# Performance work log

Measured on AMD Instinct MI355X. Metric: run time of the kernel, lower is better.

Reference implementation:

```python
import jax, jax.numpy as jnp
import numpy as np

HIDDEN = 1024
RANK = 4
INPUT = 16
ALPHA = 0.1
BASE_SCALE = 500.0
B = 32
T = 1024


def setup_inputs() -> dict:
    key = jax.random.key(0)
    k1, k2, k3, k4 = jax.random.split(key, 4)
    std = HIDDEN ** -0.25  # matches cov ~ I/sqrt(hidden) in original init
    x = jax.random.normal(k1, (B, T, INPUT), dtype=jnp.float32)
    m = jax.random.normal(k2, (HIDDEN, RANK), dtype=jnp.float32) * std
    n = jax.random.normal(k3, (HIDDEN, RANK), dtype=jnp.float32) * std
    I_mat = jax.random.normal(k4, (HIDDEN, INPUT), dtype=jnp.float32) * std
    return {"x": x, "m": m, "n": n, "I_mat": I_mat}


def reference(x, m, n, I_mat):
    # J = (m @ n.T) * base_scale / hidden ; recurrent term (J @ tanh(h).T).T
    # == tanh(h) @ J.T == ((tanh(h) @ n) @ m.T) * scale  (low-rank form, same math)
    scale = BASE_SCALE / HIDDEN

    def step(h, x_t):
        rec = (jnp.tanh(h) @ n) @ m.T * scale          # [B, H]
        dh = -h + rec + x_t @ I_mat.T                  # [B, H]
        h = h + ALPHA * dh
        return h, h

    h0 = jnp.zeros((x.shape[0], HIDDEN), dtype=x.dtype)
    _, hiddens = jax.lax.scan(step, h0, jnp.swapaxes(x, 0, 1))  # [T, B, H]
    hiddens = jnp.swapaxes(hiddens, 0, 1)                       # [B, T, H]

    span = jnp.concatenate([m, I_mat], axis=1)   # [H, RANK+INPUT]
    proj = jnp.linalg.pinv(span)                 # [RANK+INPUT, H]
    # (pinv(span) @ hiddens.permute(0,2,1)).permute(0,2,1)
    return jnp.einsum('ph,bth->btp', proj, hiddens)  # [B, T, RANK+INPUT]
```

## Files before the change

### kernel.cpp

```cpp
#include <hip/hip_runtime.h>
#include <math.h>

#define HIDDEN_ 1024
#define RANK_ 4
#define INPUT_ 16
#define T_ 1024
#define BATCH_ 32

#define NTHREADS_ 256
#define NWAVES_ (NTHREADS_ / 64)
#define EPT_ (HIDDEN_ / NTHREADS_)
#define CH_ 64
#define NCH_ (T_ / CH_)

typedef float f32x4 __attribute__((ext_vector_type(4)));

__device__ __forceinline__ float fast_exp2(float x) {
#if defined(__has_builtin)
#if __has_builtin(__builtin_amdgcn_exp2f)
    return __builtin_amdgcn_exp2f(x);
#else
    return exp2f(x);
#endif
#else
    return exp2f(x);
#endif
}

__device__ __forceinline__ float fast_rcp(float x) {
#if defined(__has_builtin)
#if __has_builtin(__builtin_amdgcn_rcpf)
    return __builtin_amdgcn_rcpf(x);
#else
    return 1.0f / x;
#endif
#else
    return 1.0f / x;
#endif
}

__device__ __forceinline__ float tanh_fast(float x) {
    float e = fast_exp2(x * 2.885390081777926815f);
    return fmaf(-2.0f, fast_rcp(e + 1.0f), 1.0f);
}

#define DPP_ADD(v, ctrl)                                                          \
    do {                                                                          \
        int _t = __builtin_amdgcn_update_dpp(0, __float_as_int(v), (ctrl), 0xf,   \
                                             0xf, true);                          \
        (v) += __int_as_float(_t);                                                \
    } while (0)

#define GLOAD16(dst, ptr)                                                         \
    asm volatile("global_load_dwordx4 %0, %1, off" : "=v"(dst) : "v"(ptr) : "memory")

__global__ __launch_bounds__(NTHREADS_)
__attribute__((amdgpu_waves_per_eu(1, 1)))
void rnn_scan_kernel(
    const float* __restrict__ x,
    const float* __restrict__ m,
    const float* __restrict__ n,
    const float* __restrict__ imat,
    float* __restrict__ out)
{
    const int b    = blockIdx.x;
    const int tid  = threadIdx.x;
    const int wave = tid >> 6;
    const int lane = tid & 63;

    const float kd   = 0.9f;
    const float krec = 0.1f * (500.0f / 1024.0f);
    const float kin  = 0.1f;

    f32x4 Iv[EPT_][4];
    f32x4 mv[EPT_];
    f32x4 nv[EPT_];
#pragma unroll
    for (int j = 0; j < EPT_; ++j) {
        const int hidx = tid * EPT_ + j;
        const float* ip = imat + hidx * INPUT_;
        GLOAD16(Iv[j][0], ip);
        GLOAD16(Iv[j][1], ip + 4);
        GLOAD16(Iv[j][2], ip + 8);
        GLOAD16(Iv[j][3], ip + 12);
        GLOAD16(mv[j], m + hidx * RANK_);
        GLOAD16(nv[j], n + hidx * RANK_);
    }
    asm volatile("s_waitcnt vmcnt(0)" ::: "memory");

    float h[EPT_];
    float mrs[EPT_][RANK_];
    float nr[EPT_][RANK_];
    float Irs[EPT_][INPUT_];
#pragma unroll
    for (int j = 0; j < EPT_; ++j) {
        h[j] = 0.0f;
#pragma unroll
        for (int r = 0; r < RANK_; ++r) {
            mrs[j][r] = krec * mv[j][r];
            nr[j][r]  = nv[j][r];
        }
#pragma unroll
        for (int q = 0; q < 4; ++q) {
#pragma unroll
            for (int e = 0; e < 4; ++e)
                Irs[j][q * 4 + e] = kin * Iv[j][q][e];
        }
    }

    __shared__ float4 part[2][NWAVES_];
    __shared__ float xs[2][CH_ * INPUT_];

    const float* xb = x + (size_t)b * T_ * INPUT_;
    float* ob = out + (size_t)b * T_ * (RANK_ + INPUT_);

    {
        float4 c0 = *(const float4*)(xb + tid * 4);
        *(float4*)&xs[0][tid * 4] = c0;
    }
    float4 xstage = *(const float4*)(xb + CH_ * INPUT_ + tid * 4);

    float y = 0.0f;
    const int yoff = (tid >= 4 && tid < 20) ? (tid - 4) : 0;

    for (int t = 0; t < T_; ++t) {
        float th[EPT_];
#pragma unroll
        for (int j = 0; j < EPT_; ++j) th[j] = tanh_fast(h[j]);

        float p0 = th[0] * nr[0][0], p1 = th[0] * nr[0][1];
        float p2 = th[0] * nr[0][2], p3 = th[0] * nr[0][3];
#pragma unroll
        for (int j = 1; j < EPT_; ++j) {
            p0 = fmaf(th[j], nr[j][0], p0);
            p1 = fmaf(th[j], nr[j][1], p1);
            p2 = fmaf(th[j], nr[j][2], p2);
            p3 = fmaf(th[j], nr[j][3], p3);
        }

        DPP_ADD(p0, 0x111); DPP_ADD(p1, 0x111); DPP_ADD(p2, 0x111); DPP_ADD(p3, 0x111);
        DPP_ADD(p0, 0x112); DPP_ADD(p1, 0x112); DPP_ADD(p2, 0x112); DPP_ADD(p3, 0x112);
        DPP_ADD(p0, 0x114); DPP_ADD(p1, 0x114); DPP_ADD(p2, 0x114); DPP_ADD(p3, 0x114);
        DPP_ADD(p0, 0x118); DPP_ADD(p1, 0x118); DPP_ADD(p2, 0x118); DPP_ADD(p3, 0x118);
        DPP_ADD(p0, 0x142); DPP_ADD(p1, 0x142); DPP_ADD(p2, 0x142); DPP_ADD(p3, 0x142);
        DPP_ADD(p0, 0x143); DPP_ADD(p1, 0x143); DPP_ADD(p2, 0x143); DPP_ADD(p3, 0x143);

        if (lane == 63) part[t & 1][wave] = make_float4(p0, p1, p2, p3);

        asm volatile("s_waitcnt lgkmcnt(0)\n\ts_barrier" ::: "memory");

        if ((t & (CH_ - 1)) == 0) {
            const int c = t >> 6;
            *(float4*)&xs[(c + 1) & 1][tid * 4] = xstage;
            const int cl = (c + 2 < NCH_) ? (c + 2) : (NCH_ - 1);
            xstage = *(const float4*)(xb + cl * CH_ * INPUT_ + tid * 4);
        }

        const float* xsp = &xs[(t >> 6) & 1][(t & 63) * INPUT_];
        const float4 xa = ((const float4*)xsp)[0];
        const float4 xbv = ((const float4*)xsp)[1];
        const float4 xc = ((const float4*)xsp)[2];
        const float4 xd = ((const float4*)xsp)[3];
        const float xyv = xsp[yoff];

        const float4 q0 = part[t & 1][0];
        const float4 q1 = part[t & 1][1];
        const float4 q2 = part[t & 1][2];
        const float4 q3 = part[t & 1][3];

        float ax[EPT_];
#pragma unroll
        for (int j = 0; j < EPT_; ++j) {
            float a = xa.x * Irs[j][0];
            float c = xa.y * Irs[j][1];
            a = fmaf(xa.z, Irs[j][2], a);   c = fmaf(xa.w, Irs[j][3], c);
            a = fmaf(xbv.x, Irs[j][4], a);  c = fmaf(xbv.y, Irs[j][5], c);
            a = fmaf(xbv.z, Irs[j][6], a);  c = fmaf(xbv.w, Irs[j][7], c);
            a = fmaf(xc.x, Irs[j][8], a);   c = fmaf(xc.y, Irs[j][9], c);
            a = fmaf(xc.z, Irs[j][10], a);  c = fmaf(xc.w, Irs[j][11], c);
            a = fmaf(xd.x, Irs[j][12], a);  c = fmaf(xd.y, Irs[j][13], c);
            a = fmaf(xd.z, Irs[j][14], a);  c = fmaf(xd.w, Irs[j][15], c);
            ax[j] = a + c;
        }

        const float s0 = (q0.x + q1.x) + (q2.x + q3.x);
        const float s1 = (q0.y + q1.y) + (q2.y + q3.y);
        const float s2 = (q0.z + q1.z) + (q2.z + q3.z);
        const float s3 = (q0.w + q1.w) + (q2.w + q3.w);

#pragma unroll
        for (int j = 0; j < EPT_; ++j) {
            float a01 = fmaf(s1, mrs[j][1], fmaf(s0, mrs[j][0], ax[j]));
            float a23 = fmaf(s3, mrs[j][3], s2 * mrs[j][2]);
            h[j] = fmaf(kd, h[j], a01 + a23);
        }

        if (tid < 20) {
            float drive;
            if (tid < 4) {
                float sv = (tid == 0) ? s0 : (tid == 1) ? s1 : (tid == 2) ? s2 : s3;
                drive = krec * sv;
            } else {
                drive = kin * xyv;
            }
            y = fmaf(kd, y, drive);
            ob[t * 20 + tid] = y;
        }
    }
}

extern "C" void kernel_launch(void* const* d_in, const int* in_sizes, int n_in,
                              void* d_out, int out_size, void* d_ws, size_t ws_size,
                              hipStream_t stream) {
    const float* x    = (const float*)d_in[0];
    const float* m    = (const float*)d_in[1];
    const float* n    = (const float*)d_in[2];
    const float* imat = (const float*)d_in[3];
    float* out = (float*)d_out;

    rnn_scan_kernel<<<dim3(BATCH_), dim3(NTHREADS_), 0, stream>>>(x, m, n, imat, out);
}
```

Measured before the change: 647.9 us.

## Precompute input projection in a parallel kernel and stream it into the scan

Adds a separate fully parallel kernel that computes the input drive x_t @ I^T for every batch row and timestep into a 128 MB workspace buffer. The sequential scan kernel then loads these values with a four-step register prefetch instead of doing 64 FMAs per thread per step. This moves work off the latency-bound serial path, at the cost of writing and re-reading a large intermediate through HBM. A fallback kernel keeps the old behaviour when the workspace is too small.

```diff
diff --git a/kernel.cpp b/kernel.cpp
--- a/kernel.cpp
+++ b/kernel.cpp
@@ -12,6 +12,10 @@
 #define EPT_ (HIDDEN_ / NTHREADS_)
 #define CH_ 64
 #define NCH_ (T_ / CH_)
+
+#define PRE_BLOCKS_ 2048
+#define ROWS_ (BATCH_ * T_)
+#define PASSES_ (ROWS_ / PRE_BLOCKS_)
 
 typedef float f32x4 __attribute__((ext_vector_type(4)));
 
@@ -51,8 +55,53 @@
         (v) += __int_as_float(_t);                                                \
     } while (0)
 
-#define GLOAD16(dst, ptr)                                                         \
-    asm volatile("global_load_dwordx4 %0, %1, off" : "=v"(dst) : "v"(ptr) : "memory")
+__global__ __launch_bounds__(NTHREADS_, 2) void precompute_u(
+    const float* __restrict__ x,
+    const float* __restrict__ imat,
+    float* __restrict__ u)
+{
+    const int tid = threadIdx.x;
+    const int bid = blockIdx.x;
+    const float kin = 0.1f;
+
+    float Ir[4][INPUT_];
+#pragma unroll
+    for (int r = 0; r < 4; ++r) {
+        const float* ip = imat + (4 * tid + r) * INPUT_;
+#pragma unroll
+        for (int q = 0; q < 4; ++q) {
+            const float4 v = *(const float4*)(ip + 4 * q);
+            Ir[r][q*4+0] = kin * v.x; Ir[r][q*4+1] = kin * v.y;
+            Ir[r][q*4+2] = kin * v.z; Ir[r][q*4+3] = kin * v.w;
+        }
+    }
+
+    for (int p = 0; p < PASSES_; ++p) {
+        const int row = p * PRE_BLOCKS_ + bid;
+        const float* xr = x + (size_t)row * INPUT_;
+        float xv[INPUT_];
+#pragma unroll
+        for (int q = 0; q < 4; ++q) {
+            const float4 v = ((const float4*)xr)[q];
+            xv[q*4+0] = v.x; xv[q*4+1] = v.y; xv[q*4+2] = v.z; xv[q*4+3] = v.w;
+        }
+        float4 acc;
+        float a[4];
+#pragma unroll
+        for (int r = 0; r < 4; ++r) {
+            float s0 = xv[0] * Ir[r][0];
+            float s1 = xv[1] * Ir[r][1];
+#pragma unroll
+            for (int i = 2; i < INPUT_; i += 2) {
+                s0 = fmaf(xv[i],     Ir[r][i],     s0);
+                s1 = fmaf(xv[i + 1], Ir[r][i + 1], s1);
+            }
+            a[r] = s0 + s1;
+        }
+        acc.x = a[0]; acc.y = a[1]; acc.z = a[2]; acc.w = a[3];
+        *(float4*)(u + (size_t)row * HIDDEN_ + 4 * tid) = acc;
+    }
+}
 
 __global__ __launch_bounds__(NTHREADS_)
 __attribute__((amdgpu_waves_per_eu(1, 1)))
@@ -60,7 +109,7 @@
     const float* __restrict__ x,
     const float* __restrict__ m,
     const float* __restrict__ n,
-    const float* __restrict__ imat,
+    const float* __restrict__ u,
     float* __restrict__ out)
 {
     const int b    = blockIdx.x;
@@ -70,48 +119,26 @@
 
     const float kd   = 0.9f;
     const float krec = 0.1f * (500.0f / 1024.0f);
-    const float kin  = 0.1f;
-
-    f32x4 Iv[EPT_][4];
-    f32x4 mv[EPT_];
-    f32x4 nv[EPT_];
-#pragma unroll
-    for (int j = 0; j < EPT_; ++j) {
-        const int hidx = tid * EPT_ + j;
-        const float* ip = imat + hidx * INPUT_;
-        GLOAD16(Iv[j][0], ip);
-        GLOAD16(Iv[j][1], ip + 4);
-        GLOAD16(Iv[j][2], ip + 8);
-        GLOAD16(Iv[j][3], ip + 12);
-        GLOAD16(mv[j], m + hidx * RANK_);
-        GLOAD16(nv[j], n + hidx * RANK_);
-    }
-    asm volatile("s_waitcnt vmcnt(0)" ::: "memory");
 
     float h[EPT_];
     float mrs[EPT_][RANK_];
     float nr[EPT_][RANK_];
-    float Irs[EPT_][INPUT_];
 #pragma unroll
     for (int j = 0; j < EPT_; ++j) {
+        const int hidx = tid * EPT_ + j;
         h[j] = 0.0f;
-#pragma unroll
-        for (int r = 0; r < RANK_; ++r) {
-            mrs[j][r] = krec * mv[j][r];
-            nr[j][r]  = nv[j][r];
-        }
-#pragma unroll
-        for (int q = 0; q < 4; ++q) {
-#pragma unroll
-            for (int e = 0; e < 4; ++e)
-                Irs[j][q * 4 + e] = kin * Iv[j][q][e];
-        }
+        const float4 mv = *(const float4*)(m + hidx * RANK_);
+        mrs[j][0] = krec * mv.x; mrs[j][1] = krec * mv.y;
+        mrs[j][2] = krec * mv.z; mrs[j][3] = krec * mv.w;
+        const float4 nv = *(const float4*)(n + hidx * RANK_);
+        nr[j][0] = nv.x; nr[j][1] = nv.y; nr[j][2] = nv.z; nr[j][3] = nv.w;
     }
 
     __shared__ float4 part[2][NWAVES_];
     __shared__ float xs[2][CH_ * INPUT_];
 
     const float* xb = x + (size_t)b * T_ * INPUT_;
+    const float* ub = u + (size_t)b * T_ * HIDDEN_ + tid * EPT_;
     float* ob = out + (size_t)b * T_ * (RANK_ + INPUT_);
 
     {
@@ -120,9 +147,15 @@
     }
     float4 xstage = *(const float4*)(xb + CH_ * INPUT_ + tid * 4);
 
+    float4 upf[4];
+#pragma unroll
+    for (int k = 0; k < 4; ++k)
+        upf[k] = *(const float4*)(ub + (size_t)k * HIDDEN_);
+
     float y = 0.0f;
     const int yoff = (tid >= 4 && tid < 20) ? (tid - 4) : 0;
 
+#pragma unroll 4
     for (int t = 0; t < T_; ++t) {
         float th[EPT_];
 #pragma unroll
@@ -156,18 +189,122 @@
             xstage = *(const float4*)(xb + cl * CH_ * INPUT_ + tid * 4);
         }
 
+        const float4 q0 = part[t & 1][0];
+        const float4 q1 = part[t & 1][1];
+        const float4 q2 = part[t & 1][2];
+        const float4 q3 = part[t & 1][3];
+        const float xyv = xs[(t >> 6) & 1][(t & 63) * INPUT_ + yoff];
+
+        const float4 uv = upf[t & 3];
+        {
+            const int tn = (t + 4 < T_) ? (t + 4) : t;
+            upf[t & 3] = *(const float4*)(ub + (size_t)tn * HIDDEN_);
+        }
+
+        const float s0 = (q0.x + q1.x) + (q2.x + q3.x);
+        const float s1 = (q0.y + q1.y) + (q2.y + q3.y);
+        const float s2 = (q0.z + q1.z) + (q2.z + q3.z);
+        const float s3 = (q0.w + q1.w) + (q2.w + q3.w);
+
+        const float uq[4] = {uv.x, uv.y, uv.z, uv.w};
+#pragma unroll
+        for (int j = 0; j < EPT_; ++j) {
+            float a01 = fmaf(s1, mrs[j][1], fmaf(s0, mrs[j][0], uq[j]));
+            float a23 = fmaf(s3, mrs[j][3], s2 * mrs[j][2]);
+            h[j] = fmaf(kd, h[j], a01 + a23);
+        }
+
+        if (tid < 20) {
+            float drive;
+            if (tid < 4) {
+                float sv = (tid == 0) ? s0 : (tid == 1) ? s1 : (tid == 2) ? s2 : s3;
+                drive = krec * sv;
+            } else {
+                drive = 0.1f * xyv;
+            }
+            y = fmaf(kd, y, drive);
+            ob[t * 20 + tid] = y;
+        }
+    }
+}
+
+__global__ __launch_bounds__(NTHREADS_)
+__attribute__((amdgpu_waves_per_eu(1, 1)))
+void rnn_scan_fallback(
+    const float* __restrict__ x, const float* __restrict__ m,
+    const float* __restrict__ n, const float* __restrict__ imat,
+    float* __restrict__ out)
+{
+    const int b    = blockIdx.x;
+    const int tid  = threadIdx.x;
+    const int wave = tid >> 6;
+    const int lane = tid & 63;
+    const float kd = 0.9f, krec = 0.1f * (500.0f / 1024.0f), kin = 0.1f;
+
+    float h[EPT_], mrs[EPT_][RANK_], nr[EPT_][RANK_], Irs[EPT_][INPUT_];
+#pragma unroll
+    for (int j = 0; j < EPT_; ++j) {
+        const int hidx = tid * EPT_ + j;
+        h[j] = 0.0f;
+        const float4 mv = *(const float4*)(m + hidx * RANK_);
+        mrs[j][0] = krec * mv.x; mrs[j][1] = krec * mv.y;
+        mrs[j][2] = krec * mv.z; mrs[j][3] = krec * mv.w;
+        const float4 nv = *(const float4*)(n + hidx * RANK_);
+        nr[j][0] = nv.x; nr[j][1] = nv.y; nr[j][2] = nv.z; nr[j][3] = nv.w;
+#pragma unroll
+        for (int q = 0; q < 4; ++q) {
+            const float4 iv = *(const float4*)(imat + hidx * INPUT_ + q * 4);
+            Irs[j][q*4+0] = kin * iv.x; Irs[j][q*4+1] = kin * iv.y;
+            Irs[j][q*4+2] = kin * iv.z; Irs[j][q*4+3] = kin * iv.w;
+        }
+    }
+    __shared__ float4 part[2][NWAVES_];
+    __shared__ float xs[2][CH_ * INPUT_];
+    const float* xb = x + (size_t)b * T_ * INPUT_;
+    float* ob = out + (size_t)b * T_ * (RANK_ + INPUT_);
+    {
+        float4 c0 = *(const float4*)(xb + tid * 4);
+        *(float4*)&xs[0][tid * 4] = c0;
+    }
+    float4 xstage = *(const float4*)(xb + CH_ * INPUT_ + tid * 4);
+    float y = 0.0f;
+    const int yoff = (tid >= 4 && tid < 20) ? (tid - 4) : 0;
+
+    for (int t = 0; t < T_; ++t) {
+        float th[EPT_];
+#pragma unroll
+        for (int j = 0; j < EPT_; ++j) th[j] = tanh_fast(h[j]);
+        float p0 = th[0] * nr[0][0], p1 = th[0] * nr[0][1];
+        float p2 = th[0] * nr[0][2], p3 = th[0] * nr[0][3];
+#pragma unroll
+        for (int j = 1; j < EPT_; ++j) {
+            p0 = fmaf(th[j], nr[j][0], p0); p1 = fmaf(th[j], nr[j][1], p1);
+            p2 = fmaf(th[j], nr[j][2], p2); p3 = fmaf(th[j], nr[j][3], p3);
+        }
+        DPP_ADD(p0, 0x111); DPP_ADD(p1, 0x111); DPP_ADD(p2, 0x111); DPP_ADD(p3, 0x111);
+        DPP_ADD(p0, 0x112); DPP_ADD(p1, 0x112); DPP_ADD(p2, 0x112); DPP_ADD(p3, 0x112);
+        DPP_ADD(p0, 0x114); DPP_ADD(p1, 0x114); DPP_ADD(p2, 0x114); DPP_ADD(p3, 0x114);
+        DPP_ADD(p0, 0x118); DPP_ADD(p1, 0x118); DPP_ADD(p2, 0x118); DPP_ADD(p3, 0x118);
+        DPP_ADD(p0, 0x142); DPP_ADD(p1, 0x142); DPP_ADD(p2, 0x142); DPP_ADD(p3, 0x142);
+        DPP_ADD(p0, 0x143); DPP_ADD(p1, 0x143); DPP_ADD(p2, 0x143); DPP_ADD(p3, 0x143);
+        if (lane == 63) part[t & 1][wave] = make_float4(p0, p1, p2, p3);
+        asm volatile("s_waitcnt lgkmcnt(0)\n\ts_barrier" ::: "memory");
+        if ((t & (CH_ - 1)) == 0) {
+            const int c = t >> 6;
+            *(float4*)&xs[(c + 1) & 1][tid * 4] = xstage;
+            const int cl = (c + 2 < NCH_) ? (c + 2) : (NCH_ - 1);
+            xstage = *(const float4*)(xb + cl * CH_ * INPUT_ + tid * 4);
+        }
         const float* xsp = &xs[(t >> 6) & 1][(t & 63) * INPUT_];
         const float4 xa = ((const float4*)xsp)[0];
         const float4 xbv = ((const float4*)xsp)[1];
         const float4 xc = ((const float4*)xsp)[2];
         const float4 xd = ((const float4*)xsp)[3];
         const float xyv = xsp[yoff];
-
         const float4 q0 = part[t & 1][0];
         const float4 q1 = part[t & 1][1];
         const float4 q2 = part[t & 1][2];
         const float4 q3 = part[t & 1][3];
-
         float ax[EPT_];
 #pragma unroll
         for (int j = 0; j < EPT_; ++j) {
@@ -182,19 +319,16 @@
             a = fmaf(xd.z, Irs[j][14], a);  c = fmaf(xd.w, Irs[j][15], c);
             ax[j] = a + c;
         }
-
         const float s0 = (q0.x + q1.x) + (q2.x + q3.x);
         const float s1 = (q0.y + q1.y) + (q2.y + q3.y);
         const float s2 = (q0.z + q1.z) + (q2.z + q3.z);
         const float s3 = (q0.w + q1.w) + (q2.w + q3.w);
-
 #pragma unroll
         for (int j = 0; j < EPT_; ++j) {
             float a01 = fmaf(s1, mrs[j][1], fmaf(s0, mrs[j][0], ax[j]));
             float a23 = fmaf(s3, mrs[j][3], s2 * mrs[j][2]);
             h[j] = fmaf(kd, h[j], a01 + a23);
         }
-
         if (tid < 20) {
             float drive;
             if (tid < 4) {
@@ -218,5 +352,12 @@
     const float* imat = (const float*)d_in[3];
     float* out = (float*)d_out;
 
-    rnn_scan_kernel<<<dim3(BATCH_), dim3(NTHREADS_), 0, stream>>>(x, m, n, imat, out);
-}
+    const size_t u_bytes = (size_t)BATCH_ * T_ * HIDDEN_ * sizeof(float);
+    if (d_ws != nullptr && ws_size >= u_bytes) {
+        float* u = (float*)d_ws;
+        precompute_u<<<dim3(PRE_BLOCKS_), dim3(NTHREADS_), 0, stream>>>(x, imat, u);
+        rnn_scan_kernel<<<dim3(BATCH_), dim3(NTHREADS_), 0, stream>>>(x, m, n, u, out);
+    } else {
+        rnn_scan_fallback<<<dim3(BATCH_), dim3(NTHREADS_), 0, stream>>>(x, m, n, imat, out);
+    }
+}
```

Result: faster. 570.4 us (-12.0%).
